# Performance work log

Hardware: AMD Instinct MI355X
Metric: run time of the kernel (lower is better)

Reference implementation:

```python
import jax, jax.numpy as jnp
import numpy as np

REG = 0.05  # reg_param > 0 -> entropic (logsumexp) branch
N, M, D = 16384, 8192, 128


def setup_inputs() -> dict:
    key = jax.random.key(0)
    k1, k2, k3 = jax.random.split(key, 3)
    source_data = jax.random.normal(k1, (N, D), dtype=jnp.float32)
    target_data = jax.random.normal(k2, (M, D), dtype=jnp.float32)
    psi = jax.random.normal(k3, (M,), dtype=jnp.float32) * 0.1
    return {"source_data": source_data, "target_data": target_data, "psi": psi}


def reference(source_data, target_data, psi):
    # squared norms
    ty2 = jnp.sum(target_data ** 2, axis=1)            # [M]
    sx2 = jnp.sum(source_data ** 2, axis=1, keepdims=True)  # [N,1]
    scale = jnp.mean(ty2)                              # scalar normalizer
    # pairwise squared-distance cost, normalized (matches torch expansion)
    cost_xy = (sx2 + ty2[None, :] - 2.0 * source_data @ target_data.T) / scale  # [N,M]
    # entropic semi-dual: -reg * logsumexp((psi - c)/reg) averaged over x
    lse = jax.nn.logsumexp((psi[None, :] - cost_xy) / REG, axis=1)  # [N]
    cte = REG * jnp.log(jnp.asarray(M, dtype=jnp.float32))
    return jnp.mean(-REG * lse) + jnp.mean(psi) + cte
```

## Files before the change

### kernel.cpp

```cpp
#include <hip/hip_runtime.h>
#include <stdint.h>

#define REG_P   0.05f
#define LOG2E   1.4426950408889634f
#define LN2     0.6931471805599453f
#define NSPLIT  16

typedef int   int32x8 __attribute__((ext_vector_type(8)));
typedef float floatx4 __attribute__((ext_vector_type(4)));

__device__ inline int32x8 load32B(const void* p) {
    union { int32x8 v; uint4 q[2]; } u;
    u.q[0] = ((const uint4*)p)[0];
    u.q[1] = ((const uint4*)p)[1];
    return u.v;
}

__device__ inline float block_sum_f(const float* __restrict__ v, int M, int tid,
                                    float* redbuf) {
    float s = 0.f;
    const float4* v4 = (const float4*)v;
    for (int j = tid; j < (M >> 2); j += 256) {
        float4 q = v4[j];
        s += (q.x + q.y) + (q.z + q.w);
    }
    #pragma unroll
    for (int mask = 1; mask < 64; mask <<= 1) s += __shfl_xor(s, mask, 64);
    int wv = tid >> 6, lane = tid & 63;
    if (lane == 0) redbuf[wv] = s;
    __syncthreads();
    return (redbuf[0] + redbuf[1]) + (redbuf[2] + redbuf[3]);
}

__global__ void k1_pack(const float* __restrict__ src, const float* __restrict__ tgt,
                        unsigned char* __restrict__ Sb8, unsigned char* __restrict__ Tbs8,
                        float* __restrict__ sx2, float* __restrict__ ty2,
                        float* __restrict__ out, int N, int M) {
    int tid = threadIdx.x;
    if (blockIdx.x == 0 && tid == 0) out[0] = 0.0f;
    int r16 = tid >> 4;
    int c8  = tid & 15;
    int row_id = blockIdx.x * 16 + r16;
    bool isS = row_id < N;
    int row = isS ? row_id : row_id - N;
    const float4* sp = (const float4*)((isS ? src : tgt) + (size_t)row * 128 + c8 * 8);
    float4 f0 = sp[0], f1 = sp[1];
    int w0 = 0, w1 = 0;
    w0 = __builtin_amdgcn_cvt_pk_fp8_f32(f0.x, f0.y, w0, false);
    w0 = __builtin_amdgcn_cvt_pk_fp8_f32(f0.z, f0.w, w0, true);
    w1 = __builtin_amdgcn_cvt_pk_fp8_f32(f1.x, f1.y, w1, false);
    w1 = __builtin_amdgcn_cvt_pk_fp8_f32(f1.z, f1.w, w1, true);
    uint2 val = make_uint2((unsigned)w0, (unsigned)w1);
    float sq = f0.x*f0.x + f0.y*f0.y + f0.z*f0.z + f0.w*f0.w
             + f1.x*f1.x + f1.y*f1.y + f1.z*f1.z + f1.w*f1.w;
    #pragma unroll
    for (int mask = 1; mask < 16; mask <<= 1) sq += __shfl_xor(sq, mask, 16);
    if (isS) {
        ((uint2*)(Sb8 + (size_t)row * 128 + c8 * 8))[0] = val;
        if (c8 == 0) sx2[row] = sq;
    } else {
        int t = row >> 6, jc = row & 63;
        int ct = jc >> 4, l16 = jc & 15;
        int quad = c8 >> 2, rem = c8 & 3;
        size_t dst = (size_t)t * 8192 + (size_t)((ct * 64 + quad * 16 + l16) * 32 + rem * 8);
        ((uint2*)(Tbs8 + dst))[0] = val;
        if (c8 == 0) ty2[row] = sq;
    }
}

__global__ __launch_bounds__(256, 4) void k3_main(
    const unsigned char* __restrict__ Sb8, const unsigned char* __restrict__ Tbs8,
    const float* __restrict__ psi, const float* __restrict__ ty2,
    float* __restrict__ lpart, int N, int M) {
    __shared__ float sb2a[512];
    __shared__ float redA[4];
    const int tid  = threadIdx.x;
    const int lane = tid & 63;
    const int wv   = tid >> 6;
    const int quad = lane >> 4, l16 = lane & 15;
    const int b = blockIdx.x;
    const int split = b & 15;
    const int i0 = (b >> 4) * 256;
    const int mspan = M / NSPLIT;
    const int jstart = split * mspan;

    float ty2sum = block_sum_f(ty2, M, tid, redA);
    float scale = ty2sum / (float)M;
    float c1 = 1.0f / (REG_P * scale);
    float a2 = 2.0f * LOG2E / (REG_P * scale);

    for (int idx = tid; idx < mspan; idx += 256) {
        int j = jstart + idx;
        sb2a[idx] = (psi[j] * (1.0f / REG_P) - ty2[j] * c1) * LOG2E;
    }
    __syncthreads();

    int32x8 afrag[4];
    #pragma unroll
    for (int rt = 0; rt < 4; ++rt)
        afrag[rt] = load32B(Sb8 + (size_t)(i0 + wv * 64 + rt * 16 + l16) * 128 + quad * 32);

    float ls[4][4];
    #pragma unroll
    for (int rt = 0; rt < 4; ++rt)
        #pragma unroll
        for (int r = 0; r < 4; ++r) ls[rt][r] = 0.0f;

    const unsigned char* gb = Tbs8 + (size_t)jstart * 128 + (size_t)lane * 32;
    const floatx4 zero4 = (floatx4){0.f, 0.f, 0.f, 0.f};
    const int SC = 0x7F7F7F7F;

    int32x8 bc = load32B(gb);
    int32x8 bn = load32B(gb + 2048);
    floatx4 accP[4];
    float bvP = 0.0f;
    bool first = true;

    #pragma unroll 4
    for (int u = 0; u < 32; ++u) {
        float bv = sb2a[u * 16 + l16];
        floatx4 a[4];
        #pragma unroll
        for (int rt = 0; rt < 4; ++rt)
            a[rt] = __builtin_amdgcn_mfma_scale_f32_16x16x128_f8f6f4(
                afrag[rt], bc, zero4, 0, 0, 0, SC, 0, SC);
        int32x8 bf = load32B(gb + (size_t)(u + 2) * 2048);
        if (!first) {
            #pragma unroll
            for (int rt = 0; rt < 4; ++rt)
                #pragma unroll
                for (int r = 0; r < 4; ++r)
                    ls[rt][r] += __builtin_amdgcn_exp2f(fmaf(a2, accP[rt][r], bvP));
        }
        #pragma unroll
        for (int rt = 0; rt < 4; ++rt) accP[rt] = a[rt];
        bvP = bv;
        bc = bn; bn = bf;
        first = false;
    }
    #pragma unroll
    for (int rt = 0; rt < 4; ++rt)
        #pragma unroll
        for (int r = 0; r < 4; ++r)
            ls[rt][r] += __builtin_amdgcn_exp2f(fmaf(a2, accP[rt][r], bvP));

    #pragma unroll
    for (int rt = 0; rt < 4; ++rt)
        #pragma unroll
        for (int r = 0; r < 4; ++r) {
            float v = ls[rt][r];
            #pragma unroll
            for (int mask = 1; mask < 16; mask <<= 1) v += __shfl_xor(v, mask, 64);
            if (l16 == 0) {
                int rowg = i0 + wv * 64 + rt * 16 + quad * 4 + r;
                lpart[(size_t)rowg * NSPLIT + split] = v;
            }
        }
}

__global__ void k4_reduce(const float* __restrict__ lpart,
                          const float* __restrict__ sx2,
                          const float* __restrict__ psi,
                          const float* __restrict__ ty2,
                          float* __restrict__ out, int N, int M) {
    __shared__ float redA[4];
    __shared__ float redB[4];
    int tid = threadIdx.x;
    float ty2s = block_sum_f(ty2, M, tid, redA);
    float scale = ty2s / (float)M;

    int i = blockIdx.x * 256 + tid;
    const float4* lp = (const float4*)(lpart + (size_t)i * NSPLIT);
    float s = 0.f;
    #pragma unroll
    for (int q = 0; q < NSPLIT / 4; ++q) {
        float4 p = lp[q];
        s += (p.x + p.y) + (p.z + p.w);
    }
    float L2 = __builtin_amdgcn_logf(s);
    float t = (-REG_P * LN2 * L2 + sx2[i] / scale) * (1.0f / (float)N);
    if (i < M) t += psi[i] * (1.0f / (float)M);
    #pragma unroll
    for (int mask = 1; mask < 64; mask <<= 1) t += __shfl_xor(t, mask, 64);
    int wv = tid >> 6, lane = tid & 63;
    if (lane == 0) redB[wv] = t;
    __syncthreads();
    if (tid == 0) {
        float total = (redB[0] + redB[1]) + (redB[2] + redB[3]);
        if (blockIdx.x == 0) total += REG_P * logf((float)M);
        atomicAdd(out, total);
    }
}

extern "C" void kernel_launch(void* const* d_in, const int* in_sizes, int n_in,
                              void* d_out, int out_size, void* d_ws, size_t ws_size,
                              hipStream_t stream) {
    const float* src = (const float*)d_in[0];
    const float* tgt = (const float*)d_in[1];
    const float* psi = (const float*)d_in[2];
    const int D = 128;
    const int N = in_sizes[0] / D;
    const int M = in_sizes[1] / D;

    char* ws = (char*)d_ws;
    float* sx2   = (float*)ws;
    float* ty2   = (float*)(ws + (size_t)N * 4);
    float* lpart = (float*)(ws + (size_t)N * 4 + (size_t)M * 4);
    size_t off = (size_t)N * 4 + (size_t)M * 4 + (size_t)N * NSPLIT * 4;
    off = (off + 255) & ~(size_t)255;
    unsigned char* Sb8  = (unsigned char*)(ws + off);
    unsigned char* Tbs8 = Sb8 + (size_t)N * 128;

    k1_pack<<<(N + M) / 16, 256, 0, stream>>>(src, tgt, Sb8, Tbs8, sx2, ty2,
                                              (float*)d_out, N, M);
    k3_main<<<(N / 256) * NSPLIT, 256, 0, stream>>>(Sb8, Tbs8, psi, ty2, lpart, N, M);
    k4_reduce<<<N / 256, 256, 0, stream>>>(lpart, sx2, psi, ty2, (float*)d_out, N, M);
}
```

Before: 97.66 us.

## Fuse final reduction into main kernel via atomics and last-block counter

```diff
diff --git a/kernel.cpp b/kernel.cpp
--- a/kernel.cpp
+++ b/kernel.cpp
@@ -35,9 +35,11 @@
 __global__ void k1_pack(const float* __restrict__ src, const float* __restrict__ tgt,
                         unsigned char* __restrict__ Sb8, unsigned char* __restrict__ Tbs8,
                         float* __restrict__ sx2, float* __restrict__ ty2,
+                        float* __restrict__ lsum, unsigned int* __restrict__ cnt,
                         float* __restrict__ out, int N, int M) {
     int tid = threadIdx.x;
     if (blockIdx.x == 0 && tid == 0) out[0] = 0.0f;
+    if (blockIdx.x < 64 && tid == 0) cnt[blockIdx.x] = 0u;
     int r16 = tid >> 4;
     int c8  = tid & 15;
     int row_id = blockIdx.x * 16 + r16;
@@ -57,7 +59,7 @@
     for (int mask = 1; mask < 16; mask <<= 1) sq += __shfl_xor(sq, mask, 16);
     if (isS) {
         ((uint2*)(Sb8 + (size_t)row * 128 + c8 * 8))[0] = val;
-        if (c8 == 0) sx2[row] = sq;
+        if (c8 == 0) { sx2[row] = sq; lsum[row] = 0.0f; }
     } else {
         int t = row >> 6, jc = row & 63;
         int ct = jc >> 4, l16 = jc & 15;
@@ -71,16 +73,20 @@
 __global__ __launch_bounds__(256, 4) void k3_main(
     const unsigned char* __restrict__ Sb8, const unsigned char* __restrict__ Tbs8,
     const float* __restrict__ psi, const float* __restrict__ ty2,
-    float* __restrict__ lpart, int N, int M) {
+    const float* __restrict__ sx2, float* __restrict__ lsum,
+    unsigned int* __restrict__ cnt, float* __restrict__ out, int N, int M) {
     __shared__ float sb2a[512];
     __shared__ float redA[4];
+    __shared__ float redB[4];
+    __shared__ int isLast;
     const int tid  = threadIdx.x;
     const int lane = tid & 63;
     const int wv   = tid >> 6;
     const int quad = lane >> 4, l16 = lane & 15;
     const int b = blockIdx.x;
     const int split = b & 15;
-    const int i0 = (b >> 4) * 256;
+    const int rowgroup = b >> 4;
+    const int i0 = rowgroup * 256;
     const int mspan = M / NSPLIT;
     const int jstart = split * mspan;
 
@@ -153,42 +159,31 @@
             for (int mask = 1; mask < 16; mask <<= 1) v += __shfl_xor(v, mask, 64);
             if (l16 == 0) {
                 int rowg = i0 + wv * 64 + rt * 16 + quad * 4 + r;
-                lpart[(size_t)rowg * NSPLIT + split] = v;
+                atomicAdd(&lsum[rowg], v);
             }
         }
-}
-
-__global__ void k4_reduce(const float* __restrict__ lpart,
-                          const float* __restrict__ sx2,
-                          const float* __restrict__ psi,
-                          const float* __restrict__ ty2,
-                          float* __restrict__ out, int N, int M) {
-    __shared__ float redA[4];
-    __shared__ float redB[4];
-    int tid = threadIdx.x;
-    float ty2s = block_sum_f(ty2, M, tid, redA);
-    float scale = ty2s / (float)M;
-
-    int i = blockIdx.x * 256 + tid;
-    const float4* lp = (const float4*)(lpart + (size_t)i * NSPLIT);
-    float s = 0.f;
-    #pragma unroll
-    for (int q = 0; q < NSPLIT / 4; ++q) {
-        float4 p = lp[q];
-        s += (p.x + p.y) + (p.z + p.w);
-    }
-    float L2 = __builtin_amdgcn_logf(s);
-    float t = (-REG_P * LN2 * L2 + sx2[i] / scale) * (1.0f / (float)N);
-    if (i < M) t += psi[i] * (1.0f / (float)M);
-    #pragma unroll
-    for (int mask = 1; mask < 64; mask <<= 1) t += __shfl_xor(t, mask, 64);
-    int wv = tid >> 6, lane = tid & 63;
-    if (lane == 0) redB[wv] = t;
+
+    __threadfence();
+    if (tid == 0) {
+        unsigned int old = atomicAdd(&cnt[rowgroup], 1u);
+        isLast = (old == NSPLIT - 1);
+    }
     __syncthreads();
-    if (tid == 0) {
-        float total = (redB[0] + redB[1]) + (redB[2] + redB[3]);
-        if (blockIdx.x == 0) total += REG_P * logf((float)M);
-        atomicAdd(out, total);
+    if (isLast) {
+        int i = i0 + tid;
+        float s = atomicAdd(&lsum[i], 0.0f);
+        float L2 = __builtin_amdgcn_logf(s);
+        float t = (-REG_P * LN2 * L2 + sx2[i] / scale) * (1.0f / (float)N);
+        if (i < M) t += psi[i] * (1.0f / (float)M);
+        #pragma unroll
+        for (int mask = 1; mask < 64; mask <<= 1) t += __shfl_xor(t, mask, 64);
+        if (lane == 0) redB[wv] = t;
+        __syncthreads();
+        if (tid == 0) {
+            float total = (redB[0] + redB[1]) + (redB[2] + redB[3]);
+            if (rowgroup == 0) total += REG_P * logf((float)M);
+            atomicAdd(out, total);
+        }
     }
 }
 
@@ -205,14 +200,15 @@
     char* ws = (char*)d_ws;
     float* sx2   = (float*)ws;
     float* ty2   = (float*)(ws + (size_t)N * 4);
-    float* lpart = (float*)(ws + (size_t)N * 4 + (size_t)M * 4);
-    size_t off = (size_t)N * 4 + (size_t)M * 4 + (size_t)N * NSPLIT * 4;
+    float* lsum  = (float*)(ws + (size_t)N * 4 + (size_t)M * 4);
+    unsigned int* cnt = (unsigned int*)(ws + (size_t)N * 8 + (size_t)M * 4);
+    size_t off = (size_t)N * 8 + (size_t)M * 4 + 256;
     off = (off + 255) & ~(size_t)255;
     unsigned char* Sb8  = (unsigned char*)(ws + off);
     unsigned char* Tbs8 = Sb8 + (size_t)N * 128;
 
     k1_pack<<<(N + M) / 16, 256, 0, stream>>>(src, tgt, Sb8, Tbs8, sx2, ty2,
-                                              (float*)d_out, N, M);
-    k3_main<<<(N / 256) * NSPLIT, 256, 0, stream>>>(Sb8, Tbs8, psi, ty2, lpart, N, M);
-    k4_reduce<<<N / 256, 256, 0, stream>>>(lpart, sx2, psi, ty2, (float*)d_out, N, M);
-}
+                                              lsum, cnt, (float*)d_out, N, M);
+    k3_main<<<(N / 256) * NSPLIT, 256, 0, stream>>>(Sb8, Tbs8, psi, ty2, sx2,
+                                                    lsum, cnt, (float*)d_out, N, M);
+}
```

Measured after the change: 145.8 us. 1.49x slower.
